# Performance work log

Measured on AMD Instinct MI355X. Metric: run time of the kernel, lower is better.

## Reference

```python
import jax, jax.numpy as jnp
import numpy as np

B, N, D_IN, D_OUT = 8, 2048, 256, 128
ROW_ZERO = 85 - 10  # hardcoded in original: a[:, 0:85-10] = 0 (zeros rows, dim 1)
NEG_BIG = -9.0e15
EPS = 1e-12  # F.normalize eps


def setup_inputs() -> dict:
    key = jax.random.key(0)
    k1, k2, k3, k4 = jax.random.split(key, 4)
    h = jax.random.normal(k1, (B, N, D_IN), dtype=jnp.float32)
    adj = jax.random.randint(k2, (B, N, N), 0, 2, dtype=jnp.int32)
    adj_eye = jax.random.randint(k3, (B, N, N), 0, 2, dtype=jnp.int32)
    # xavier_uniform with gain=1.414 for W [in, out]
    limit = 1.414 * np.sqrt(6.0 / (D_IN + D_OUT))
    W = jax.random.uniform(k4, (D_IN, D_OUT), minval=-limit, maxval=limit, dtype=jnp.float32)
    return {"h": h, "adj": adj, "adj_eye": adj_eye, "W": W}


def reference(h, adj, adj_eye, W):
    # Wh: [B, N, D_OUT]
    Wh = jnp.matmul(h, W)
    # L2-normalize along feature dim (F.normalize semantics: x / max(||x||, eps))
    norm = jnp.maximum(jnp.linalg.norm(Wh, axis=-1, keepdims=True), EPS)
    Whn = Wh / norm
    # dense cosine-similarity scores: [B, N, N]
    score = jnp.einsum("bnd,bmd->bnm", Whn, Whn)
    # double-sort top-k emulation (faithful to original, incl. row-wise zeroing bug)
    a_sorted = jnp.sort(score, axis=-1)
    idx1 = jnp.argsort(score, axis=-1)
    a_sorted = a_sorted.at[:, 0:ROW_ZERO, :].set(0.0)
    idx2 = jnp.argsort(idx1, axis=-1)  # inverse permutation
    attscore = jnp.take_along_axis(a_sorted, idx2, axis=-1)
    # adjacency mask + softmax over neighbors
    e = jnp.where(adj_eye > 0, attscore, NEG_BIG)
    attention = jax.nn.softmax(e, axis=-1)
    # (dropout is identity in eval mode)
    h_prime = jnp.matmul(attention, Wh)
    return jax.nn.elu(h_prime)
```

## Files before the change

### kernel.cpp

```cpp
#include <hip/hip_runtime.h>
#include <stdint.h>

#define NN   2048
#define DD   128
#define DIN  256
#define ROWZ 75

typedef float f32x4 __attribute__((ext_vector_type(4)));
typedef short bf16x8 __attribute__((ext_vector_type(8)));
typedef int   i32x2  __attribute__((ext_vector_type(2)));
typedef unsigned int u32x2 __attribute__((ext_vector_type(2)));

__device__ __forceinline__ unsigned short f2bf(float x){
  union { float f; unsigned int u; } v; v.f = x;
  unsigned int u = v.u;
  u += 0x7fffu + ((u >> 16) & 1u);
  return (unsigned short)(u >> 16);
}

__launch_bounds__(256, 2)
__global__ void wh_kernel(const float* __restrict__ h, const float* __restrict__ W,
                          unsigned short* __restrict__ whn, unsigned short* __restrict__ whT)
{
  __shared__ float hs[32][36];
  __shared__ float Ws[32][128];
  __shared__ float ssp[32][33];
  __shared__ float sinv[32];

  const int t  = threadIdx.x;
  const int bid = blockIdx.x;
  const int r0 = ((bid & 7) << 11) | ((bid >> 3) << 5);
  const int r4 = (t >> 5) * 4;
  const int d4 = (t & 31) * 4;

  float acc[4][4];
#pragma unroll
  for (int i = 0; i < 4; ++i)
#pragma unroll
    for (int j = 0; j < 4; ++j) acc[i][j] = 0.f;

  const int lrow = t >> 3;
  const int lkb  = (t & 7) * 4;
  const int wk   = t >> 3;
  const int wd   = (t & 7) * 16;

  f32x4 ph = *(const f32x4*)(h + (size_t)(r0 + lrow) * DIN + lkb);
  f32x4 pW[4];
  {
    const float* ws = W + (size_t)wk * DD + wd;
#pragma unroll
    for (int e = 0; e < 4; ++e) pW[e] = ((const f32x4*)ws)[e];
  }

  for (int kt = 0; kt < 8; ++kt){
    __syncthreads();
#pragma unroll
    for (int e = 0; e < 4; ++e) hs[lkb + e][lrow] = ph[e];
    {
      f32x4* dst = (f32x4*)&Ws[wk][wd];
#pragma unroll
      for (int e = 0; e < 4; ++e) dst[e] = pW[e];
    }
    __syncthreads();

    if (kt < 7){
      ph = *(const f32x4*)(h + (size_t)(r0 + lrow) * DIN + (kt+1)*32 + lkb);
      const float* ws = W + (size_t)((kt+1)*32 + wk) * DD + wd;
#pragma unroll
      for (int e = 0; e < 4; ++e) pW[e] = ((const f32x4*)ws)[e];
    }

#pragma unroll
    for (int k = 0; k < 32; ++k){
      f32x4 w4 = *(const f32x4*)&Ws[k][d4];
      f32x4 ha = *(const f32x4*)&hs[k][r4];
#pragma unroll
      for (int i = 0; i < 4; ++i)
#pragma unroll
        for (int j = 0; j < 4; ++j)
          acc[i][j] += ha[i] * w4[j];
    }
  }

#pragma unroll
  for (int i = 0; i < 4; ++i){
    float s = acc[i][0]*acc[i][0] + acc[i][1]*acc[i][1]
            + acc[i][2]*acc[i][2] + acc[i][3]*acc[i][3];
    ssp[r4 + i][t & 31] = s;
  }
  __syncthreads();
  if (t < 32){
    float ss = 0.f;
#pragma unroll
    for (int c = 0; c < 32; ++c) ss += ssp[t][c];
    sinv[t] = 1.0f / fmaxf(sqrtf(ss), 1e-12f);
  }
  __syncthreads();

  const int bb = r0 >> 11;
  const int n0 = (r0 & 2047) + r4;

#pragma unroll
  for (int i = 0; i < 4; ++i){
    const float inv = sinv[r4 + i];
    unsigned int lo = (unsigned int)f2bf(acc[i][0]*inv) | ((unsigned int)f2bf(acc[i][1]*inv) << 16);
    unsigned int hi = (unsigned int)f2bf(acc[i][2]*inv) | ((unsigned int)f2bf(acc[i][3]*inv) << 16);
    u32x2 pk = { lo, hi };
    *(u32x2*)(whn + (size_t)(r0 + r4 + i) * DD + d4) = pk;
  }
#pragma unroll
  for (int j = 0; j < 4; ++j){
    u32x2 pk;
#pragma unroll
    for (int e = 0; e < 2; ++e)
      pk[e] = (unsigned int)f2bf(acc[2*e][j]) | ((unsigned int)f2bf(acc[2*e + 1][j]) << 16);
    *(u32x2*)(whT + ((size_t)(bb * DD + d4 + j)) * NN + n0) = pk;
  }
}

__launch_bounds__(512, 2)
__global__ void attn_kernel(const unsigned short* __restrict__ whn,
                            const unsigned short* __restrict__ whT,
                            const int* __restrict__ adje,
                            float* __restrict__ out)
{
  __shared__ float smem[16384];
  __shared__ float linv_s[64];

  const int t    = threadIdx.x;
  const int w    = t >> 6;
  const int l    = t & 63;
  const int quad = l >> 4;
  const int l16  = l & 15;
  const int qh   = w >> 2;
  const int ms   = w & 3;
  const int b     = blockIdx.x & 7;
  const int qbase = (blockIdx.x >> 3) * 64;

  const unsigned short* whn_b = whn + (size_t)b * NN * DD;
  const unsigned short* whT_b = whT + (size_t)b * DD * NN;
  const int*            adj_b = adje + (size_t)b * NN * NN;

  unsigned short* const Pw = (unsigned short*)smem + w * (32 * 40);

  bf16x8 qf[2][4];
#pragma unroll
  for (int s = 0; s < 2; ++s)
#pragma unroll
    for (int kc = 0; kc < 4; ++kc)
      qf[s][kc] = *(const bf16x8*)(whn_b + (size_t)(qbase + qh*32 + s*16 + l16) * DD + kc*32 + quad*8);

  f32x4 oacc[2][8];
  float lacc[2][4];
#pragma unroll
  for (int s = 0; s < 2; ++s){
#pragma unroll
    for (int dt = 0; dt < 8; ++dt) oacc[s][dt] = (f32x4){0.f, 0.f, 0.f, 0.f};
#pragma unroll
    for (int r = 0; r < 4; ++r) lacc[s][r] = 0.f;
  }

  bool zr[2][4];
#pragma unroll
  for (int s = 0; s < 2; ++s)
#pragma unroll
    for (int r = 0; r < 4; ++r)
      zr[s][r] = (qbase + qh*32 + s*16 + quad*4 + r) < ROWZ;

  i32x2 av[2][4];
#pragma unroll
  for (int s = 0; s < 2; ++s)
#pragma unroll
    for (int r = 0; r < 4; ++r)
      av[s][r] = *(const i32x2*)(adj_b + (size_t)(qbase + qh*32 + s*16 + quad*4 + r) * NN + ms*32 + 2*l16);

  for (int it = 0; it < 16; ++it){
    const int m0 = it * 128;

    bf16x8 kf[2][4];
#pragma unroll
    for (int f = 0; f < 2; ++f)
#pragma unroll
      for (int kc = 0; kc < 4; ++kc)
        kf[f][kc] = *(const bf16x8*)(whn_b + (size_t)(m0 + ms*32 + 2*l16 + f) * DD + kc*32 + quad*8);

    i32x2 avn[2][4];
    if (it < 15){
      const int mn = m0 + 128;
#pragma unroll
      for (int s = 0; s < 2; ++s)
#pragma unroll
        for (int r = 0; r < 4; ++r)
          avn[s][r] = *(const i32x2*)(adj_b + (size_t)(qbase + qh*32 + s*16 + quad*4 + r) * NN + mn + ms*32 + 2*l16);
    }

#pragma unroll
    for (int s = 0; s < 2; ++s){
      f32x4 sc0 = (f32x4){0.f,0.f,0.f,0.f};
      f32x4 sc1 = (f32x4){0.f,0.f,0.f,0.f};
#pragma unroll
      for (int kc = 0; kc < 4; ++kc){
        sc0 = __builtin_amdgcn_mfma_f32_16x16x32_bf16(qf[s][kc], kf[0][kc], sc0, 0, 0, 0);
        sc1 = __builtin_amdgcn_mfma_f32_16x16x32_bf16(qf[s][kc], kf[1][kc], sc1, 0, 0, 0);
      }
#pragma unroll
      for (int r = 0; r < 4; ++r){
        float sv0 = zr[s][r] ? 0.f : sc0[r];
        float sv1 = zr[s][r] ? 0.f : sc1[r];
        float p0 = (av[s][r].x > 0) ? __expf(sv0) : 0.f;
        float p1 = (av[s][r].y > 0) ? __expf(sv1) : 0.f;
        lacc[s][r] += p0 + p1;
        unsigned int pk = (unsigned int)f2bf(p0) | ((unsigned int)f2bf(p1) << 16);
        *(unsigned int*)&Pw[(s*16 + quad*4 + r) * 40 + 2*l16] = pk;
      }
    }

    bf16x8 pfr0 = *(const bf16x8*)&Pw[(l16) * 40 + quad*8];
    bf16x8 pfr1 = *(const bf16x8*)&Pw[(16 + l16) * 40 + quad*8];
    bf16x8 vf[8];
#pragma unroll
    for (int dt = 0; dt < 8; ++dt)
      vf[dt] = *(const bf16x8*)(whT_b + (size_t)(dt*16 + l16) * NN + m0 + ms*32 + quad*8);
    __builtin_amdgcn_s_setprio(1);
#pragma unroll
    for (int dt = 0; dt < 8; ++dt){
      oacc[0][dt] = __builtin_amdgcn_mfma_f32_16x16x32_bf16(pfr0, vf[dt], oacc[0][dt], 0, 0, 0);
      oacc[1][dt] = __builtin_amdgcn_mfma_f32_16x16x32_bf16(pfr1, vf[dt], oacc[1][dt], 0, 0, 0);
    }
    __builtin_amdgcn_s_setprio(0);

#pragma unroll
    for (int s = 0; s < 2; ++s)
#pragma unroll
      for (int r = 0; r < 4; ++r)
        av[s][r] = avn[s][r];
  }

  __syncthreads();

  {
    float* fl = smem;
#pragma unroll
    for (int s = 0; s < 2; ++s)
#pragma unroll
      for (int r = 0; r < 4; ++r)
        fl[(qh*32 + s*16 + quad*4 + r) * 64 + ms*16 + l16] = lacc[s][r];
  }
  __syncthreads();
  if (t < 64){
    const float* fl = smem;
    float sum = 0.f;
#pragma unroll
    for (int c = 0; c < 64; ++c) sum += fl[t * 64 + c];
    linv_s[t] = 1.0f / sum;
  }

  float* const owf = smem;
  for (int s = 0; s < 2; ++s){
    __syncthreads();
#pragma unroll
    for (int dt = 0; dt < 8; ++dt)
#pragma unroll
      for (int r = 0; r < 4; ++r)
        owf[w*2048 + (quad*4 + r)*128 + dt*16 + l16] = oacc[s][dt][r];
    __syncthreads();
#pragma unroll
    for (int j = 0; j < 8; ++j){
      const int o     = j*512 + t;
      const int row32 = o >> 7;
      const int d     = o & 127;
      const int qh2   = row32 >> 4;
      const int r16   = row32 & 15;
      float v = owf[(qh2*4 + 0)*2048 + r16*128 + d]
              + owf[(qh2*4 + 1)*2048 + r16*128 + d]
              + owf[(qh2*4 + 2)*2048 + r16*128 + d]
              + owf[(qh2*4 + 3)*2048 + r16*128 + d];
      const int qrl = qh2*32 + s*16 + r16;
      v *= linv_s[qrl];
      v = (v > 0.f) ? v : expm1f(v);
      out[(size_t)(b*NN + qbase + qrl) * DD + d] = v;
    }
  }
}

extern "C" void kernel_launch(void* const* d_in, const int* in_sizes, int n_in,
                              void* d_out, int out_size, void* d_ws, size_t ws_size,
                              hipStream_t stream)
{
  const float* h       = (const float*)d_in[0];
  const int*   adj_eye = (const int*)d_in[2];
  const float* W       = (const float*)d_in[3];
  float*       out     = (float*)d_out;

  unsigned short* whn  = (unsigned short*)d_ws;
  unsigned short* whT  = whn + (size_t)16384 * 128;

  wh_kernel<<<512, 256, 0, stream>>>(h, W, whn, whT);
  attn_kernel<<<256, 512, 0, stream>>>(whn, whT, adj_eye, out);
}
```

Measured before the change: 319.0 us.

## Halve query tile, split key range across 8 waves, bitpack adjacency in LDS

The attention kernel now handles 32 query rows per block instead of 64, doubling the grid to 512 blocks. All 8 waves share the same queries and split the key range among themselves. Each block preloads its adjacency rows with wide vector loads and packs them into 32-bit masks in shared memory, replacing the per-iteration strided int loads and the register prefetch. The Wh kernel uses 512 threads with 2 rows per thread. Together these aim to raise occupancy and make adjacency reads more coalesced, at the cost of reading each key/value tile twice as often across blocks and a larger 8-way cross-wave reduction.

Result: slower. 380.1 us (+19.2%).

```diff
diff --git a/kernel.cpp b/kernel.cpp
--- a/kernel.cpp
+++ b/kernel.cpp
@@ -6,9 +6,10 @@
 #define DIN  256
 #define ROWZ 75
 
+typedef float f32x2 __attribute__((ext_vector_type(2)));
 typedef float f32x4 __attribute__((ext_vector_type(4)));
 typedef short bf16x8 __attribute__((ext_vector_type(8)));
-typedef int   i32x2  __attribute__((ext_vector_type(2)));
+typedef int   i32x4  __attribute__((ext_vector_type(4)));
 typedef unsigned int u32x2 __attribute__((ext_vector_type(2)));
 
 __device__ __forceinline__ unsigned short f2bf(float x){
@@ -18,7 +19,7 @@
   return (unsigned short)(u >> 16);
 }
 
-__launch_bounds__(256, 2)
+__launch_bounds__(512, 4)
 __global__ void wh_kernel(const float* __restrict__ h, const float* __restrict__ W,
                           unsigned short* __restrict__ whn, unsigned short* __restrict__ whT)
 {
@@ -27,55 +28,54 @@
   __shared__ float ssp[32][33];
   __shared__ float sinv[32];
 
-  const int t  = threadIdx.x;
+  const int t   = threadIdx.x;
   const int bid = blockIdx.x;
-  const int r0 = ((bid & 7) << 11) | ((bid >> 3) << 5);
-  const int r4 = (t >> 5) * 4;
-  const int d4 = (t & 31) * 4;
-
-  float acc[4][4];
-#pragma unroll
-  for (int i = 0; i < 4; ++i)
+  const int r0  = ((bid & 7) << 11) | ((bid >> 3) << 5);
+  const int r2  = (t >> 5) * 2;
+  const int d4  = (t & 31) * 4;
+
+  float acc[2][4];
+#pragma unroll
+  for (int i = 0; i < 2; ++i)
 #pragma unroll
     for (int j = 0; j < 4; ++j) acc[i][j] = 0.f;
 
-  const int lrow = t >> 3;
-  const int lkb  = (t & 7) * 4;
-  const int wk   = t >> 3;
-  const int wd   = (t & 7) * 16;
-
-  f32x4 ph = *(const f32x4*)(h + (size_t)(r0 + lrow) * DIN + lkb);
-  f32x4 pW[4];
+  const int hrow = t >> 4;
+  const int hk   = (t & 15) * 2;
+  const int wk   = t >> 4;
+  const int wd   = (t & 15) * 8;
+
+  f32x2 ph = *(const f32x2*)(h + (size_t)(r0 + hrow) * DIN + hk);
+  f32x4 pW0, pW1;
   {
     const float* ws = W + (size_t)wk * DD + wd;
-#pragma unroll
-    for (int e = 0; e < 4; ++e) pW[e] = ((const f32x4*)ws)[e];
+    pW0 = ((const f32x4*)ws)[0];
+    pW1 = ((const f32x4*)ws)[1];
   }
 
   for (int kt = 0; kt < 8; ++kt){
     __syncthreads();
-#pragma unroll
-    for (int e = 0; e < 4; ++e) hs[lkb + e][lrow] = ph[e];
+    hs[hk][hrow]     = ph.x;
+    hs[hk + 1][hrow] = ph.y;
     {
       f32x4* dst = (f32x4*)&Ws[wk][wd];
-#pragma unroll
-      for (int e = 0; e < 4; ++e) dst[e] = pW[e];
+      dst[0] = pW0; dst[1] = pW1;
     }
     __syncthreads();
 
     if (kt < 7){
-      ph = *(const f32x4*)(h + (size_t)(r0 + lrow) * DIN + (kt+1)*32 + lkb);
+      ph = *(const f32x2*)(h + (size_t)(r0 + hrow) * DIN + (kt+1)*32 + hk);
       const float* ws = W + (size_t)((kt+1)*32 + wk) * DD + wd;
-#pragma unroll
-      for (int e = 0; e < 4; ++e) pW[e] = ((const f32x4*)ws)[e];
+      pW0 = ((const f32x4*)ws)[0];
+      pW1 = ((const f32x4*)ws)[1];
     }
 
 #pragma unroll
     for (int k = 0; k < 32; ++k){
       f32x4 w4 = *(const f32x4*)&Ws[k][d4];
-      f32x4 ha = *(const f32x4*)&hs[k][r4];
-#pragma unroll
-      for (int i = 0; i < 4; ++i)
+      f32x2 ha = *(const f32x2*)&hs[k][r2];
+#pragma unroll
+      for (int i = 0; i < 2; ++i)
 #pragma unroll
         for (int j = 0; j < 4; ++j)
           acc[i][j] += ha[i] * w4[j];
@@ -83,10 +83,10 @@
   }
 
 #pragma unroll
-  for (int i = 0; i < 4; ++i){
+  for (int i = 0; i < 2; ++i){
     float s = acc[i][0]*acc[i][0] + acc[i][1]*acc[i][1]
             + acc[i][2]*acc[i][2] + acc[i][3]*acc[i][3];
-    ssp[r4 + i][t & 31] = s;
+    ssp[r2 + i][t & 31] = s;
   }
   __syncthreads();
   if (t < 32){
@@ -98,57 +98,69 @@
   __syncthreads();
 
   const int bb = r0 >> 11;
-  const int n0 = (r0 & 2047) + r4;
-
-#pragma unroll
-  for (int i = 0; i < 4; ++i){
-    const float inv = sinv[r4 + i];
+  const int n0 = (r0 & 2047) + r2;
+
+#pragma unroll
+  for (int i = 0; i < 2; ++i){
+    const float inv = sinv[r2 + i];
     unsigned int lo = (unsigned int)f2bf(acc[i][0]*inv) | ((unsigned int)f2bf(acc[i][1]*inv) << 16);
     unsigned int hi = (unsigned int)f2bf(acc[i][2]*inv) | ((unsigned int)f2bf(acc[i][3]*inv) << 16);
     u32x2 pk = { lo, hi };
-    *(u32x2*)(whn + (size_t)(r0 + r4 + i) * DD + d4) = pk;
+    *(u32x2*)(whn + (size_t)(r0 + r2 + i) * DD + d4) = pk;
   }
 #pragma unroll
   for (int j = 0; j < 4; ++j){
-    u32x2 pk;
-#pragma unroll
-    for (int e = 0; e < 2; ++e)
-      pk[e] = (unsigned int)f2bf(acc[2*e][j]) | ((unsigned int)f2bf(acc[2*e + 1][j]) << 16);
-    *(u32x2*)(whT + ((size_t)(bb * DD + d4 + j)) * NN + n0) = pk;
-  }
-}
-
-__launch_bounds__(512, 2)
+    unsigned int pk = (unsigned int)f2bf(acc[0][j]) | ((unsigned int)f2bf(acc[1][j]) << 16);
+    *(unsigned int*)(whT + ((size_t)(bb * DD + d4 + j)) * NN + n0) = pk;
+  }
+}
+
+__launch_bounds__(512, 4)
 __global__ void attn_kernel(const unsigned short* __restrict__ whn,
                             const unsigned short* __restrict__ whT,
                             const int* __restrict__ adje,
                             float* __restrict__ out)
 {
   __shared__ float smem[16384];
-  __shared__ float linv_s[64];
+  __shared__ float linv_s[32];
 
   const int t    = threadIdx.x;
   const int w    = t >> 6;
   const int l    = t & 63;
   const int quad = l >> 4;
   const int l16  = l & 15;
-  const int qh   = w >> 2;
-  const int ms   = w & 3;
+  const int ms   = w;
   const int b     = blockIdx.x & 7;
-  const int qbase = (blockIdx.x >> 3) * 64;
+  const int qbase = (blockIdx.x >> 3) * 32;
 
   const unsigned short* whn_b = whn + (size_t)b * NN * DD;
   const unsigned short* whT_b = whT + (size_t)b * DD * NN;
   const int*            adj_b = adje + (size_t)b * NN * NN;
 
   unsigned short* const Pw = (unsigned short*)smem + w * (32 * 40);
+  unsigned int*   const Mk = (unsigned int*)smem + 5120;
+
+  for (int rr = 0; rr < 4; ++rr){
+    const int row = w*4 + rr;
+    const int* src = adj_b + (size_t)(qbase + row) * NN + l*32;
+    i32x4 c[8];
+#pragma unroll
+    for (int j = 0; j < 8; ++j) c[j] = *(const i32x4*)(src + j*4);
+    unsigned int m = 0;
+#pragma unroll
+    for (int j = 0; j < 8; ++j)
+#pragma unroll
+      for (int e = 0; e < 4; ++e)
+        m |= (unsigned int)(c[j][e] > 0) << (j*4 + e);
+    Mk[row*65 + l] = m;
+  }
 
   bf16x8 qf[2][4];
 #pragma unroll
   for (int s = 0; s < 2; ++s)
 #pragma unroll
     for (int kc = 0; kc < 4; ++kc)
-      qf[s][kc] = *(const bf16x8*)(whn_b + (size_t)(qbase + qh*32 + s*16 + l16) * DD + kc*32 + quad*8);
+      qf[s][kc] = *(const bf16x8*)(whn_b + (size_t)(qbase + s*16 + l16) * DD + kc*32 + quad*8);
 
   f32x4 oacc[2][8];
   float lacc[2][4];
@@ -165,17 +177,12 @@
   for (int s = 0; s < 2; ++s)
 #pragma unroll
     for (int r = 0; r < 4; ++r)
-      zr[s][r] = (qbase + qh*32 + s*16 + quad*4 + r) < ROWZ;
-
-  i32x2 av[2][4];
-#pragma unroll
-  for (int s = 0; s < 2; ++s)
-#pragma unroll
-    for (int r = 0; r < 4; ++r)
-      av[s][r] = *(const i32x2*)(adj_b + (size_t)(qbase + qh*32 + s*16 + quad*4 + r) * NN + ms*32 + 2*l16);
-
-  for (int it = 0; it < 16; ++it){
-    const int m0 = it * 128;
+      zr[s][r] = (qbase + s*16 + quad*4 + r) < ROWZ;
+
+  __syncthreads();
+
+  for (int it = 0; it < 8; ++it){
+    const int m0 = it * 256;
 
     bf16x8 kf[2][4];
 #pragma unroll
@@ -184,15 +191,12 @@
       for (int kc = 0; kc < 4; ++kc)
         kf[f][kc] = *(const bf16x8*)(whn_b + (size_t)(m0 + ms*32 + 2*l16 + f) * DD + kc*32 + quad*8);
 
-    i32x2 avn[2][4];
-    if (it < 15){
-      const int mn = m0 + 128;
-#pragma unroll
-      for (int s = 0; s < 2; ++s)
-#pragma unroll
-        for (int r = 0; r < 4; ++r)
-          avn[s][r] = *(const i32x2*)(adj_b + (size_t)(qbase + qh*32 + s*16 + quad*4 + r) * NN + mn + ms*32 + 2*l16);
-    }
+    unsigned int aw[2][4];
+#pragma unroll
+    for (int s = 0; s < 2; ++s)
+#pragma unroll
+      for (int r = 0; r < 4; ++r)
+        aw[s][r] = Mk[(s*16 + quad*4 + r)*65 + it*8 + ms];
 
 #pragma unroll
     for (int s = 0; s < 2; ++s){
@@ -207,8 +211,8 @@
       for (int r = 0; r < 4; ++r){
         float sv0 = zr[s][r] ? 0.f : sc0[r];
         float sv1 = zr[s][r] ? 0.f : sc1[r];
-        float p0 = (av[s][r].x > 0) ? __expf(sv0) : 0.f;
-        float p1 = (av[s][r].y > 0) ? __expf(sv1) : 0.f;
+        float p0 = ((aw[s][r] >> (2*l16    )) & 1u) ? __expf(sv0) : 0.f;
+        float p1 = ((aw[s][r] >> (2*l16 + 1)) & 1u) ? __expf(sv1) : 0.f;
         lacc[s][r] += p0 + p1;
         unsigned int pk = (unsigned int)f2bf(p0) | ((unsigned int)f2bf(p1) << 16);
         *(unsigned int*)&Pw[(s*16 + quad*4 + r) * 40 + 2*l16] = pk;
@@ -228,12 +232,6 @@
       oacc[1][dt] = __builtin_amdgcn_mfma_f32_16x16x32_bf16(pfr1, vf[dt], oacc[1][dt], 0, 0, 0);
     }
     __builtin_amdgcn_s_setprio(0);
-
-#pragma unroll
-    for (int s = 0; s < 2; ++s)
-#pragma unroll
-      for (int r = 0; r < 4; ++r)
-        av[s][r] = avn[s][r];
   }
 
   __syncthreads();
@@ -244,14 +242,14 @@
     for (int s = 0; s < 2; ++s)
 #pragma unroll
       for (int r = 0; r < 4; ++r)
-        fl[(qh*32 + s*16 + quad*4 + r) * 64 + ms*16 + l16] = lacc[s][r];
-  }
-  __syncthreads();
-  if (t < 64){
+        fl[(s*16 + quad*4 + r) * 132 + w*16 + l16] = lacc[s][r];
+  }
+  __syncthreads();
+  if (t < 32){
     const float* fl = smem;
     float sum = 0.f;
 #pragma unroll
-    for (int c = 0; c < 64; ++c) sum += fl[t * 64 + c];
+    for (int c = 0; c < 128; ++c) sum += fl[t * 132 + c];
     linv_s[t] = 1.0f / sum;
   }
 
@@ -265,17 +263,15 @@
         owf[w*2048 + (quad*4 + r)*128 + dt*16 + l16] = oacc[s][dt][r];
     __syncthreads();
 #pragma unroll
-    for (int j = 0; j < 8; ++j){
-      const int o     = j*512 + t;
-      const int row32 = o >> 7;
-      const int d     = o & 127;
-      const int qh2   = row32 >> 4;
-      const int r16   = row32 & 15;
-      float v = owf[(qh2*4 + 0)*2048 + r16*128 + d]
-              + owf[(qh2*4 + 1)*2048 + r16*128 + d]
-              + owf[(qh2*4 + 2)*2048 + r16*128 + d]
-              + owf[(qh2*4 + 3)*2048 + r16*128 + d];
-      const int qrl = qh2*32 + s*16 + r16;
+    for (int j = 0; j < 4; ++j){
+      const int o   = j*512 + t;
+      const int r16 = o >> 7;
+      const int d   = o & 127;
+      float v = 0.f;
+#pragma unroll
+      for (int ww = 0; ww < 8; ++ww)
+        v += owf[ww*2048 + r16*128 + d];
+      const int qrl = s*16 + r16;
       v *= linv_s[qrl];
       v = (v > 0.f) ? v : expm1f(v);
       out[(size_t)(b*NN + qbase + qrl) * DD + d] = v;
@@ -295,6 +291,6 @@
   unsigned short* whn  = (unsigned short*)d_ws;
   unsigned short* whT  = whn + (size_t)16384 * 128;
 
-  wh_kernel<<<512, 256, 0, stream>>>(h, W, whn, whT);
-  attn_kernel<<<256, 512, 0, stream>>>(whn, whT, adj_eye, out);
-}
+  wh_kernel<<<512, 512, 0, stream>>>(h, W, whn, whT);
+  attn_kernel<<<512, 512, 0, stream>>>(whn, whT, adj_eye, out);
+}
```
